# Kernel optimization log

Measured on AMD Instinct MI355X. Metric: run time of the kernel, lower is better.

## Reference

```python
import jax, jax.numpy as jnp
import numpy as np

N = 50000      # nodes
E = 600000     # directed edges (before self-loops)
IN, HID, OUT = 512, 128, 40
EPS_BN = 1e-5
DROP_P = 0.5   # hardcoded in forward via BernoulliDropout(0.5)

# BinActive: sign() forward, straight-through estimator backward (|x|<=1 gate)
@jax.custom_vjp
def binactive(x):
    return jnp.sign(x)

def _ba_fwd(x):
    return jnp.sign(x), x

def _ba_bwd(x, g):
    return (g * (jnp.abs(x) <= 1.0).astype(g.dtype),)

binactive.defvjp(_ba_fwd, _ba_bwd)


def setup_inputs() -> dict:
    key = jax.random.key(0)
    ks = jax.random.split(key, 8)
    x = jax.random.normal(ks[0], (N, IN), dtype=jnp.float32)
    edge_index = jax.random.randint(ks[1], (2, E), 0, N, dtype=jnp.int64)
    w0 = jax.random.normal(ks[2], (IN, HID), dtype=jnp.float32) * 0.05
    b0 = jnp.zeros((HID,), jnp.float32)
    w1 = jax.random.normal(ks[3], (HID, HID), dtype=jnp.float32) * 0.05
    b1 = jnp.zeros((HID,), jnp.float32)
    w2 = jax.random.normal(ks[4], (HID, OUT), dtype=jnp.float32) * 0.05
    b2 = jnp.zeros((OUT,), jnp.float32)
    return {"x": x, "edge_index": edge_index,
            "w0": w0, "b0": b0, "w1": w1, "b1": b1, "w2": w2, "b2": b2}


def _gcn_norm(edge_index):
    # add self-loops, compute symmetric normalization deg^-1/2 A deg^-1/2
    loops = jnp.arange(N, dtype=edge_index.dtype)
    row = jnp.concatenate([edge_index[0], loops])  # destinations
    col = jnp.concatenate([edge_index[1], loops])  # sources
    deg = jax.ops.segment_sum(jnp.ones_like(row, dtype=jnp.float32), row, num_segments=N)
    dinv = jnp.where(deg > 0, deg ** -0.5, 0.0)
    norm = dinv[row] * dinv[col]                   # [E+N]
    return row, col, norm


def _gcn_conv(x, w, b, row, col, norm):
    # binarized weight: sign(w) scaled by mean(|w|) (XNOR-style)
    wb = binactive(w) * jnp.mean(jnp.abs(w))
    h = x @ wb                                     # [N, out]
    msg = h[col] * norm[:, None]                   # gather + scale
    agg = jax.ops.segment_sum(msg, row, num_segments=N)
    return agg + b


def reference(x, edge_index, w0, b0, w1, b1, w2, b2):
    # BatchNorm1d(affine=False), training-mode batch stats over nodes
    mean = jnp.mean(x, axis=0)
    var = jnp.var(x, axis=0)
    h = (x - mean) / jnp.sqrt(var + EPS_BN)

    row, col, norm = _gcn_norm(edge_index)
    dkey = jax.random.key(42)
    weights = [(w0, b0), (w1, b1), (w2, b2)]
    n_layers = len(weights)
    for i, (w, b) in enumerate(weights):
        h = binactive(h)
        h = _gcn_conv(h, w, b, row, col, norm)
        if i != n_layers - 1:  # BernoulliDropout(0.5)
            mask = jax.random.bernoulli(jax.random.fold_in(dkey, i), 1.0 - DROP_P, h.shape)
            h = h * mask.astype(h.dtype) * (1.0 / (1.0 - DROP_P))
    return jax.nn.log_softmax(h, axis=1)
```

## Files before the change

### kernel.cpp

```cpp
#include <hip/hip_runtime.h>
#include <stdint.h>
#include <stddef.h>

#define NN 50000
#define NE 600000
#define DI 512
#define DH 128
#define DO 40
#define MTOT (NN * DH)
#define NBLK ((NN + 255) / 256)
#define CSB 400
#define GEMMB ((NN / 16 + 3) / 4)
#define DEG4B ((NE / 4 + 255) / 256)

using int4v = __attribute__((ext_vector_type(4))) int;

__host__ __device__ inline uint32_t rotl32(uint32_t v, int d) {
  return (v << d) | (v >> (32 - d));
}

__host__ __device__ inline void threefry2x32(uint32_t k0, uint32_t k1,
                                             uint32_t c0, uint32_t c1,
                                             uint32_t* o0, uint32_t* o1) {
  uint32_t ks0 = k0, ks1 = k1, ks2 = k0 ^ k1 ^ 0x1BD11BDAu;
  uint32_t x0 = c0 + ks0, x1 = c1 + ks1;
  const int R0[4] = {13, 15, 26, 6};
  const int R1[4] = {17, 29, 16, 24};
#define TF_R4(R) { x0 += x1; x1 = rotl32(x1, R[0]); x1 ^= x0; \
                   x0 += x1; x1 = rotl32(x1, R[1]); x1 ^= x0; \
                   x0 += x1; x1 = rotl32(x1, R[2]); x1 ^= x0; \
                   x0 += x1; x1 = rotl32(x1, R[3]); x1 ^= x0; }
  TF_R4(R0); x0 += ks1; x1 += ks2 + 1u;
  TF_R4(R1); x0 += ks2; x1 += ks0 + 2u;
  TF_R4(R0); x0 += ks0; x1 += ks1 + 3u;
  TF_R4(R1); x0 += ks1; x1 += ks2 + 4u;
  TF_R4(R0); x0 += ks2; x1 += ks0 + 5u;
#undef TF_R4
  *o0 = x0; *o1 = x1;
}

__device__ inline void colsum_body(const float* __restrict__ x,
                                   double* __restrict__ colsum, int blk) {
  const int t = threadIdx.x;
  const int grp = blk >> 1;
  const int col = ((blk & 1) << 8) + t;
  const float* xp = x + (size_t)grp * 250 * DI + col;
  double s = 0.0;
  for (int i = 0; i < 10; ++i) {
    float f0  = xp[0 * DI],  f1  = xp[1 * DI],  f2  = xp[2 * DI];
    float f3  = xp[3 * DI],  f4  = xp[4 * DI],  f5  = xp[5 * DI];
    float f6  = xp[6 * DI],  f7  = xp[7 * DI],  f8  = xp[8 * DI];
    float f9  = xp[9 * DI],  f10 = xp[10 * DI], f11 = xp[11 * DI];
    float f12 = xp[12 * DI], f13 = xp[13 * DI], f14 = xp[14 * DI];
    float f15 = xp[15 * DI], f16 = xp[16 * DI], f17 = xp[17 * DI];
    float f18 = xp[18 * DI], f19 = xp[19 * DI], f20 = xp[20 * DI];
    float f21 = xp[21 * DI], f22 = xp[22 * DI], f23 = xp[23 * DI];
    float f24 = xp[24 * DI];
    asm volatile("" :: "v"(f0), "v"(f1), "v"(f2), "v"(f3), "v"(f4),
                       "v"(f5), "v"(f6), "v"(f7), "v"(f8), "v"(f9),
                       "v"(f10), "v"(f11), "v"(f12), "v"(f13), "v"(f14),
                       "v"(f15), "v"(f16), "v"(f17), "v"(f18), "v"(f19),
                       "v"(f20), "v"(f21), "v"(f22), "v"(f23), "v"(f24));
    s += (double)f0;  s += (double)f1;  s += (double)f2;  s += (double)f3;
    s += (double)f4;  s += (double)f5;  s += (double)f6;  s += (double)f7;
    s += (double)f8;  s += (double)f9;  s += (double)f10; s += (double)f11;
    s += (double)f12; s += (double)f13; s += (double)f14; s += (double)f15;
    s += (double)f16; s += (double)f17; s += (double)f18; s += (double)f19;
    s += (double)f20; s += (double)f21; s += (double)f22; s += (double)f23;
    s += (double)f24;
    xp += 25 * DI;
  }
  unsafeAtomicAdd(&colsum[col], s);
}

__device__ inline void wfuse_body(const float* __restrict__ w,
                                  uint32_t* __restrict__ frag,
                                  double* __restrict__ slot,
                                  int K, int C, int NT, int blk,
                                  double* red) {
  int steps = K >> 6;
  int total = steps * NT * 64 * 4;
  int idx = blk * 256 + threadIdx.x;
  double a = 0.0;
  if (idx < total) {
    int dw = idx & 3;
    int lane = (idx >> 2) & 63;
    int rest = idx >> 8;
    int t = rest % NT;
    int s = rest / NT;
    int n = t * 16 + (lane & 15);
    int kbase = s * 64 + (lane >> 4) * 16 + dw * 4;
    uint32_t v = 0;
    if (n < C) {
#pragma unroll
      for (int j = 0; j < 4; ++j) {
        float wv = w[(size_t)(kbase + j) * C + n];
        uint32_t sg = (uint8_t)(int8_t)((wv > 0.f) ? 1 : ((wv < 0.f) ? -1 : 0));
        v |= sg << (8 * j);
        a += (double)fabsf(wv);
      }
    }
    frag[idx] = v;
  }
  red[threadIdx.x] = a;
  __syncthreads();
  for (int ofs = 128; ofs > 0; ofs >>= 1) {
    if (threadIdx.x < ofs) red[threadIdx.x] += red[threadIdx.x + ofs];
    __syncthreads();
  }
  if (threadIdx.x == 0) unsafeAtomicAdd(slot, red[0]);
}

__global__ void prologue_fused(const float* __restrict__ x,
                               double* __restrict__ colsum,
                               const int* __restrict__ ei,
                               uint32_t* __restrict__ deg,
                               const float* __restrict__ w0,
                               const float* __restrict__ w1,
                               const float* __restrict__ w2,
                               uint32_t* __restrict__ f0,
                               uint32_t* __restrict__ f1,
                               uint32_t* __restrict__ f2,
                               double* __restrict__ slots) {
  __shared__ double red[256];
  int b = blockIdx.x;
  if (b < CSB) {
    colsum_body(x, colsum, b);
  } else if (b < CSB + DEG4B) {
    int idx = (b - CSB) * 256 + threadIdx.x;
    if (idx < NE / 4) {
      int4 d4 = *(const int4*)(ei + 4 * idx);
      atomicAdd(&deg[d4.x], 1u);
      atomicAdd(&deg[d4.y], 1u);
      atomicAdd(&deg[d4.z], 1u);
      atomicAdd(&deg[d4.w], 1u);
    }
  } else {
    int wb = b - (CSB + DEG4B);
    if (wb < 64)       wfuse_body(w0, f0, slots + 0, DI, DH, 8, wb,      red);
    else if (wb < 80)  wfuse_body(w1, f1, slots + 1, DH, DH, 8, wb - 64, red);
    else               wfuse_body(w2, f2, slots + 2, DH, DO, 3, wb - 80, red);
  }
}

__global__ void scan_mean(const uint32_t* __restrict__ deg,
                          uint32_t* __restrict__ rowptr,
                          uint32_t* __restrict__ bsum,
                          double* __restrict__ dinv,
                          double* __restrict__ colsum) {
  __shared__ uint32_t bs[256];
  int b = blockIdx.x;
  int t = threadIdx.x;
  if (b < NBLK) {
    int i = b * 256 + t;
    uint32_t v = (i < NN) ? deg[i] : 0u;
    if (i < NN) dinv[i] = 1.0 / sqrt((double)(v + 1u));
    bs[t] = v;
    __syncthreads();
    for (int ofs = 1; ofs < 256; ofs <<= 1) {
      uint32_t add = (t >= ofs) ? bs[t - ofs] : 0u;
      __syncthreads();
      bs[t] += add;
      __syncthreads();
    }
    if (i < NN) rowptr[i] = bs[t] - v;
    if (t == 255) bsum[b] = bs[255];
  } else {
    int c = (b - NBLK) * 256 + t;
    if (c < DI) colsum[c] = colsum[c] / (double)NN;
  }
}

__global__ void scan_bsum(const uint32_t* __restrict__ bsum,
                          uint32_t* __restrict__ base) {
  __shared__ uint32_t bs[256];
  int t = threadIdx.x;
  uint32_t v = (t < NBLK) ? bsum[t] : 0u;
  bs[t] = v;
  __syncthreads();
  for (int ofs = 1; ofs < 256; ofs <<= 1) {
    uint32_t add = (t >= ofs) ? bs[t - ofs] : 0u;
    __syncthreads();
    bs[t] += add;
    __syncthreads();
  }
  if (t < NBLK) base[t] = bs[t] - v;
}

__global__ void csr_gemm0(const int* __restrict__ ei,
                          const uint32_t* __restrict__ rowptr,
                          const uint32_t* __restrict__ base,
                          uint32_t* __restrict__ cursor,
                          int* __restrict__ csr_src,
                          const float* __restrict__ x,
                          const double* __restrict__ mean,
                          const uint32_t* __restrict__ frag,
                          int8_t* __restrict__ H) {
  if (blockIdx.x < DEG4B) {
    int idx = blockIdx.x * 256 + threadIdx.x;
    if (idx < NE / 4) {
      int4 d4 = *(const int4*)(ei + 4 * idx);
      int4 s4 = *(const int4*)(ei + NE + 4 * idx);
      uint32_t p0 = rowptr[d4.x] + base[d4.x >> 8] + atomicAdd(&cursor[d4.x], 1u);
      uint32_t p1 = rowptr[d4.y] + base[d4.y >> 8] + atomicAdd(&cursor[d4.y], 1u);
      uint32_t p2 = rowptr[d4.z] + base[d4.z >> 8] + atomicAdd(&cursor[d4.z], 1u);
      uint32_t p3 = rowptr[d4.w] + base[d4.w >> 8] + atomicAdd(&cursor[d4.w], 1u);
      csr_src[p0] = s4.x;
      csr_src[p1] = s4.y;
      csr_src[p2] = s4.z;
      csr_src[p3] = s4.w;
    }
    return;
  }
  const int blk = blockIdx.x - DEG4B;
  const uint4* fg = (const uint4*)frag;
  const int lane = threadIdx.x & 63;
  const int wv = threadIdx.x >> 6;
  const int r0 = (blk * 4 + wv) * 16;
  if (r0 >= NN) return;
  const int m = lane & 15, q = lane >> 4;
  const float* xp = x + (size_t)(r0 + m) * DI + q * 16;
  const double* mp0 = mean + q * 16;
  int4v acc[8];
#pragma unroll
  for (int t = 0; t < 8; ++t) acc[t] = (int4v){0, 0, 0, 0};
#pragma unroll
  for (int s = 0; s < 8; ++s) {
    const float* xs = xp + s * 64;
    const double* mp = mp0 + s * 64;
    int4v a;
#pragma unroll
    for (int w4 = 0; w4 < 4; ++w4) {
      float4 f = *(const float4*)(xs + 4 * w4);
      double v0 = (double)f.x - mp[4 * w4 + 0];
      double v1 = (double)f.y - mp[4 * w4 + 1];
      double v2 = (double)f.z - mp[4 * w4 + 2];
      double v3 = (double)f.w - mp[4 * w4 + 3];
      uint32_t o = 0;
      o |= (uint8_t)(int8_t)((v0 > 0.0) ? 1 : ((v0 < 0.0) ? -1 : 0));
      o |= ((uint32_t)(uint8_t)(int8_t)((v1 > 0.0) ? 1 : ((v1 < 0.0) ? -1 : 0))) << 8;
      o |= ((uint32_t)(uint8_t)(int8_t)((v2 > 0.0) ? 1 : ((v2 < 0.0) ? -1 : 0))) << 16;
      o |= ((uint32_t)(uint8_t)(int8_t)((v3 > 0.0) ? 1 : ((v3 < 0.0) ? -1 : 0))) << 24;
      a[w4] = (int)o;
    }
#pragma unroll
    for (int t = 0; t < 8; ++t) {
      int4v b = *(const int4v*)&fg[(s * 8 + t) * 64 + lane];
      acc[t] = __builtin_amdgcn_mfma_i32_16x16x64_i8(a, b, acc[t], 0, 0, 0);
    }
  }
  int8_t* hp = H + (size_t)r0 * DH;
#pragma unroll
  for (int t = 0; t < 8; ++t) {
    int n = t * 16 + m;
#pragma unroll
    for (int r = 0; r < 4; ++r)
      hp[(size_t)(q * 4 + r) * DH + n] = (int8_t)(acc[t][r] >> 1);
  }
}

template <int STEPS, int NT, int C, int SHIFT>
__global__ void gemm_mfma(const int8_t* __restrict__ S,
                          const uint32_t* __restrict__ frag,
                          int8_t* __restrict__ H) {
  extern __shared__ uint4 lb[];
  const int tot = STEPS * NT * 64;
  const uint4* fg = (const uint4*)frag;
  for (int i = threadIdx.x; i < tot; i += 256) lb[i] = fg[i];
  __syncthreads();
  const int lane = threadIdx.x & 63;
  const int wv = threadIdx.x >> 6;
  const int r0 = (blockIdx.x * 4 + wv) * 16;
  if (r0 >= NN) return;
  const int m = lane & 15, q = lane >> 4;
  const int K = STEPS * 64;
  const int8_t* sp = S + (size_t)(r0 + m) * K + q * 16;
  int4v acc[NT];
#pragma unroll
  for (int t = 0; t < NT; ++t) acc[t] = (int4v){0, 0, 0, 0};
#pragma unroll
  for (int s = 0; s < STEPS; ++s) {
    int4v a = *(const int4v*)(sp + (size_t)s * 64);
#pragma unroll
    for (int t = 0; t < NT; ++t) {
      int4v b = *(const int4v*)&lb[(s * NT + t) * 64 + lane];
      acc[t] = __builtin_amdgcn_mfma_i32_16x16x64_i8(a, b, acc[t], 0, 0, 0);
    }
  }
  int8_t* hp = H + (size_t)r0 * C;
#pragma unroll
  for (int t = 0; t < NT; ++t) {
    int n = t * 16 + m;
    if (n < C) {
#pragma unroll
      for (int r = 0; r < 4; ++r)
        hp[(size_t)(q * 4 + r) * C + n] = (int8_t)(acc[t][r] >> SHIFT);
    }
  }
}

__global__ void gather128(const uint32_t* __restrict__ rowptr,
                          const uint32_t* __restrict__ base,
                          const int* __restrict__ csr_src,
                          const double* __restrict__ dinv,
                          const int8_t* __restrict__ H,
                          const float* __restrict__ b,
                          int8_t* __restrict__ Sout,
                          const double* __restrict__ wsum, double cnt,
                          uint32_t fk0, uint32_t fk1) {
  int d = (int)(((size_t)blockIdx.x * blockDim.x + threadIdx.x) >> 6);
  int lane = threadIdx.x & 63;
  if (d >= NN) return;
  const int g = lane >> 5, p = lane & 31;
  double a0 = 0.0, a1 = 0.0, a2 = 0.0, a3 = 0.0;
  const uint32_t e0 = rowptr[d] + base[d >> 8];
  const uint32_t e1 = (d + 1 < NN) ? (rowptr[d + 1] + base[(d + 1) >> 8]) : NE;
  const int L = (int)(e1 - e0) + 1;
  for (int c0 = 0; c0 < L; c0 += 64) {
    const int n = min(64, L - c0);
    const int my = c0 + lane;
    int sidx = d;
    if (my > 0 && my < L) sidx = csr_src[e0 + my - 1];
    double wv = dinv[sidx];
    int t = 0;
    {
      int sA = 0, sB = 0; double wA = 0.0, wB = 0.0;
      uint32_t hA = 0, hB = 0;
      if (4 <= n) {
        sA = __shfl(sidx, g);      wA = __shfl(wv, g);
        sB = __shfl(sidx, 2 + g);  wB = __shfl(wv, 2 + g);
        hA = *(const uint32_t*)(H + (size_t)sA * DH + 4 * p);
        hB = *(const uint32_t*)(H + (size_t)sB * DH + 4 * p);
      }
      for (; t + 4 <= n; t += 4) {
        const uint32_t cA = hA, cB = hB;
        const double vA = wA, vB = wB;
        if (t + 8 <= n) {
          sA = __shfl(sidx, t + 4 + g);  wA = __shfl(wv, t + 4 + g);
          sB = __shfl(sidx, t + 6 + g);  wB = __shfl(wv, t + 6 + g);
          hA = *(const uint32_t*)(H + (size_t)sA * DH + 4 * p);
          hB = *(const uint32_t*)(H + (size_t)sB * DH + 4 * p);
        }
        a0 += vA * (double)(int8_t)(cA);
        a1 += vA * (double)(int8_t)(cA >> 8);
        a2 += vA * (double)(int8_t)(cA >> 16);
        a3 += vA * (double)(int8_t)(cA >> 24);
        a0 += vB * (double)(int8_t)(cB);
        a1 += vB * (double)(int8_t)(cB >> 8);
        a2 += vB * (double)(int8_t)(cB >> 16);
        a3 += vB * (double)(int8_t)(cB >> 24);
      }
    }
    for (; t < n; t += 2) {
      const int j = t + g;
      const bool on = (j < n);
      const int jc = on ? j : 0;
      int s = __shfl(sidx, jc);
      double w = __shfl(wv, jc);
      w = on ? w : 0.0;
      uint32_t hv = *(const uint32_t*)(H + (size_t)s * DH + 4 * p);
      a0 += w * (double)(int8_t)(hv);
      a1 += w * (double)(int8_t)(hv >> 8);
      a2 += w * (double)(int8_t)(hv >> 16);
      a3 += w * (double)(int8_t)(hv >> 24);
    }
  }
  a0 += __shfl_xor(a0, 32);
  a1 += __shfl_xor(a1, 32);
  a2 += __shfl_xor(a2, 32);
  a3 += __shfl_xor(a3, 32);
  double sc = (wsum[0] / cnt) * dinv[d];
  int ch = 4 * p + 2 * g;
  int j0 = d * DH + ch;
  double va = sc * ((g == 0) ? a0 : a2) + (double)b[ch];
  double vb = sc * ((g == 0) ? a1 : a3) + (double)b[ch + 1];
  int s0 = (va > 0.0) ? 1 : ((va < 0.0) ? -1 : 0);
  int s1 = (vb > 0.0) ? 1 : ((vb < 0.0) ? -1 : 0);
  uint32_t r0, r1, bits0, bits1;
  threefry2x32(fk0, fk1, 0u, (uint32_t)j0, &r0, &r1);
  bits0 = r0 ^ r1;
  threefry2x32(fk0, fk1, 0u, (uint32_t)(j0 + 1), &r0, &r1);
  bits1 = r0 ^ r1;
  float u0 = __uint_as_float((bits0 >> 9) | 0x3f800000u) - 1.0f;
  float u1 = __uint_as_float((bits1 >> 9) | 0x3f800000u) - 1.0f;
  uint8_t o0 = (u0 < 0.5f) ? (uint8_t)(int8_t)s0 : (uint8_t)0;
  uint8_t o1 = (u1 < 0.5f) ? (uint8_t)(int8_t)s1 : (uint8_t)0;
  *(uint16_t*)(Sout + j0) = (uint16_t)(o0 | ((uint16_t)o1 << 8));
}

__global__ void gather40_lsm(const uint32_t* __restrict__ rowptr,
                             const uint32_t* __restrict__ base,
                             const int* __restrict__ csr_src,
                             const double* __restrict__ dinv,
                             const int8_t* __restrict__ H,
                             const float* __restrict__ b2,
                             const double* __restrict__ wsum,
                             float* __restrict__ out) {
  int d = (int)(((size_t)blockIdx.x * blockDim.x + threadIdx.x) >> 6);
  int lane = threadIdx.x & 63;
  if (d >= NN) return;
  const int g = lane >> 5, p = lane & 31;
  const bool act = (p < 20);
  double a0 = 0.0, a1 = 0.0;
  const uint32_t e0 = rowptr[d] + base[d >> 8];
  const uint32_t e1 = (d + 1 < NN) ? (rowptr[d + 1] + base[(d + 1) >> 8]) : NE;
  const int L = (int)(e1 - e0) + 1;
  for (int c0 = 0; c0 < L; c0 += 64) {
    const int n = min(64, L - c0);
    const int my = c0 + lane;
    int sidx = d;
    if (my > 0 && my < L) sidx = csr_src[e0 + my - 1];
    double wv = dinv[sidx];
    int t = 0;
    {
      int sA = 0, sB = 0; double wA = 0.0, wB = 0.0;
      uint16_t hA = 0, hB = 0;
      if (4 <= n) {
        sA = __shfl(sidx, g);      wA = __shfl(wv, g);
        sB = __shfl(sidx, 2 + g);  wB = __shfl(wv, 2 + g);
        if (act) {
          hA = *(const uint16_t*)(H + (size_t)sA * DO + 2 * p);
          hB = *(const uint16_t*)(H + (size_t)sB * DO + 2 * p);
        }
      }
      for (; t + 4 <= n; t += 4) {
        const uint16_t cA = hA, cB = hB;
        const double vA = wA, vB = wB;
        if (t + 8 <= n) {
          sA = __shfl(sidx, t + 4 + g);  wA = __shfl(wv, t + 4 + g);
          sB = __shfl(sidx, t + 6 + g);  wB = __shfl(wv, t + 6 + g);
          if (act) {
            hA = *(const uint16_t*)(H + (size_t)sA * DO + 2 * p);
            hB = *(const uint16_t*)(H + (size_t)sB * DO + 2 * p);
          }
        }
        if (act) {
          a0 += vA * (double)(int8_t)(cA);
          a1 += vA * (double)(int8_t)(cA >> 8);
          a0 += vB * (double)(int8_t)(cB);
          a1 += vB * (double)(int8_t)(cB >> 8);
        }
      }
    }
    for (; t < n; t += 2) {
      const int j = t + g;
      const bool on = (j < n);
      const int jc = on ? j : 0;
      int s = __shfl(sidx, jc);
      double w = __shfl(wv, jc);
      w = on ? w : 0.0;
      if (act) {
        uint16_t hv = *(const uint16_t*)(H + (size_t)s * DO + 2 * p);
        a0 += w * (double)(int8_t)(hv);
        a1 += w * (double)(int8_t)(hv >> 8);
      }
    }
  }
  a0 += __shfl_xor(a0, 32);
  a1 += __shfl_xor(a1, 32);
  double sc = (wsum[0] / (double)(DH * DO)) * dinv[d];
  const bool lead = (g == 0) && act;
  double v0 = 0.0, v1 = 0.0;
  if (act) {
    v0 = sc * a0 + (double)b2[2 * p];
    v1 = sc * a1 + (double)b2[2 * p + 1];
  }
  double mx = lead ? fmax(v0, v1) : -1.0e300;
  for (int ofs = 32; ofs > 0; ofs >>= 1) mx = fmax(mx, __shfl_xor(mx, ofs));
  float ex = lead ? (expf((float)(v0 - mx)) + expf((float)(v1 - mx))) : 0.f;
  for (int ofs = 32; ofs > 0; ofs >>= 1) ex += __shfl_xor(ex, ofs);
  float l = logf(ex);
  if (lead) {
    float2 o = make_float2((float)(v0 - mx) - l, (float)(v1 - mx) - l);
    *(float2*)(out + (size_t)d * DO + 2 * p) = o;
  }
}

extern "C" void kernel_launch(void* const* d_in, const int* in_sizes, int n_in,
                              void* d_out, int out_size, void* d_ws, size_t ws_size,
                              hipStream_t stream) {
  (void)in_sizes; (void)n_in; (void)out_size; (void)ws_size;
  const float* x  = (const float*)d_in[0];
  const int*   ei = (const int*)d_in[1];
  const float* w0 = (const float*)d_in[2];
  const float* b0 = (const float*)d_in[3];
  const float* w1 = (const float*)d_in[4];
  const float* b1 = (const float*)d_in[5];
  const float* w2 = (const float*)d_in[6];
  const float* b2 = (const float*)d_in[7];
  float* out = (float*)d_out;

  char* wsb = (char*)d_ws;
  double*   mean_d = (double*)wsb;
  double*   wsum_d = (double*)(wsb + 4096);
  uint32_t* deg_e  = (uint32_t*)(wsb + 4224);
  uint32_t* cursor = (uint32_t*)(wsb + 204224);
  size_t cur = 404480;
  uint32_t* rowptr = (uint32_t*)(wsb + cur); cur += 200064;
  double*   dinv_d = (double*)(wsb + cur);  cur += 400000;
  cur = (cur + 255) & ~255ull;
  uint32_t* bsum = (uint32_t*)(wsb + cur); cur += 1024;
  uint32_t* base = (uint32_t*)(wsb + cur); cur += 1024;
  int*    csr_src = (int*)(wsb + cur);    cur += (size_t)NE * 4;
  cur = (cur + 255) & ~255ull;
  uint32_t* FR0 = (uint32_t*)(wsb + cur); cur += 8 * 8 * 64 * 16;
  uint32_t* FR1 = (uint32_t*)(wsb + cur); cur += 2 * 8 * 64 * 16;
  uint32_t* FR2 = (uint32_t*)(wsb + cur); cur += 2 * 3 * 64 * 16;
  int8_t* S1  = (int8_t*)(wsb + cur); cur += (size_t)MTOT;
  cur = (cur + 255) & ~255ull;
  int8_t* H8 = (int8_t*)(wsb + cur); cur += (size_t)MTOT;

  uint32_t fkA0, fkA1, fkB0, fkB1;
  threefry2x32(0u, 42u, 0u, 0u, &fkA0, &fkA1);
  threefry2x32(0u, 42u, 0u, 1u, &fkB0, &fkB1);

  hipMemsetAsync(wsb, 0, 404224, stream);

  prologue_fused<<<CSB + DEG4B + 86, 256, 0, stream>>>(
      x, mean_d, ei, deg_e, w0, w1, w2, FR0, FR1, FR2, wsum_d);
  scan_mean<<<NBLK + 2, 256, 0, stream>>>(deg_e, rowptr, bsum, dinv_d, mean_d);
  scan_bsum<<<1, 256, 0, stream>>>(bsum, base);

  const int node_blocks = (NN * 64) / 256 + 1;
  const size_t sh1 = 2 * 8 * 64 * 16;
  const size_t sh2 = 2 * 3 * 64 * 16;

  csr_gemm0<<<DEG4B + GEMMB, 256, 0, stream>>>(ei, rowptr, base, cursor,
                                               csr_src, x, mean_d, FR0, H8);
  gather128<<<node_blocks, 256, 0, stream>>>(rowptr, base, csr_src, dinv_d, H8,
                                             b0, S1, wsum_d + 0,
                                             (double)(DI * DH / 2), fkA0, fkA1);

  gemm_mfma<2, 8, DH, 0><<<GEMMB, 256, sh1, stream>>>(S1, FR1, H8);
  gather128<<<node_blocks, 256, 0, stream>>>(rowptr, base, csr_src, dinv_d, H8,
                                             b1, S1, wsum_d + 1,
                                             (double)(DH * DH), fkB0, fkB1);

  gemm_mfma<2, 3, DO, 0><<<GEMMB, 256, sh2, stream>>>(S1, FR2, H8);
  gather40_lsm<<<node_blocks, 256, 0, stream>>>(rowptr, base, csr_src, dinv_d,
                                                H8, b2, wsum_d + 2, out);
}
```

Baseline: 369.4 us.

## Prefetch x rows in GEMM, hoist dropout RNG, load dinv per edge directly

In the int8 MFMA GEMM fused with BN-sign, x rows are loaded into a four-stage register buffer ahead of use, so global loads overlap the sign/pack and MFMA work. In gather128, the threefry dropout bits are computed before the edge loop so that ALU work can overlap the first memory latencies. In both gather kernels, the per-edge dinv weight is now read from memory (a uniform address per half-wave) instead of being broadcast with a double-precision shuffle, which removes shuffle instructions but adds dependent loads. Register pressure rises from the prefetch buffer and the hoisted RNG values.

```diff
diff --git a/kernel.cpp b/kernel.cpp
--- a/kernel.cpp
+++ b/kernel.cpp
@@ -221,21 +221,34 @@
   const int m = lane & 15, q = lane >> 4;
   const float* xp = x + (size_t)(r0 + m) * DI + q * 16;
   const double* mp0 = mean + q * 16;
+  float4 buf[4][4];
+#pragma unroll
+  for (int s = 0; s < 4; ++s)
+#pragma unroll
+    for (int w = 0; w < 4; ++w)
+      buf[s][w] = *(const float4*)(xp + s * 64 + 4 * w);
   int4v acc[8];
 #pragma unroll
   for (int t = 0; t < 8; ++t) acc[t] = (int4v){0, 0, 0, 0};
 #pragma unroll
   for (int s = 0; s < 8; ++s) {
-    const float* xs = xp + s * 64;
+    float4 f[4];
+#pragma unroll
+    for (int w = 0; w < 4; ++w) f[w] = buf[s & 3][w];
+    if (s + 4 < 8) {
+#pragma unroll
+      for (int w = 0; w < 4; ++w)
+        buf[s & 3][w] = *(const float4*)(xp + (s + 4) * 64 + 4 * w);
+    }
     const double* mp = mp0 + s * 64;
     int4v a;
 #pragma unroll
     for (int w4 = 0; w4 < 4; ++w4) {
-      float4 f = *(const float4*)(xs + 4 * w4);
-      double v0 = (double)f.x - mp[4 * w4 + 0];
-      double v1 = (double)f.y - mp[4 * w4 + 1];
-      double v2 = (double)f.z - mp[4 * w4 + 2];
-      double v3 = (double)f.w - mp[4 * w4 + 3];
+      float4 fv = f[w4];
+      double v0 = (double)fv.x - mp[4 * w4 + 0];
+      double v1 = (double)fv.y - mp[4 * w4 + 1];
+      double v2 = (double)fv.z - mp[4 * w4 + 2];
+      double v3 = (double)fv.w - mp[4 * w4 + 3];
       uint32_t o = 0;
       o |= (uint8_t)(int8_t)((v0 > 0.0) ? 1 : ((v0 < 0.0) ? -1 : 0));
       o |= ((uint32_t)(uint8_t)(int8_t)((v1 > 0.0) ? 1 : ((v1 < 0.0) ? -1 : 0))) << 8;
@@ -312,6 +325,15 @@
   int lane = threadIdx.x & 63;
   if (d >= NN) return;
   const int g = lane >> 5, p = lane & 31;
+  const int ch = 4 * p + 2 * g;
+  const int j0 = d * DH + ch;
+  uint32_t r0_, r1_, bits0, bits1;
+  threefry2x32(fk0, fk1, 0u, (uint32_t)j0, &r0_, &r1_);
+  bits0 = r0_ ^ r1_;
+  threefry2x32(fk0, fk1, 0u, (uint32_t)(j0 + 1), &r0_, &r1_);
+  bits1 = r0_ ^ r1_;
+  float u0 = __uint_as_float((bits0 >> 9) | 0x3f800000u) - 1.0f;
+  float u1 = __uint_as_float((bits1 >> 9) | 0x3f800000u) - 1.0f;
   double a0 = 0.0, a1 = 0.0, a2 = 0.0, a3 = 0.0;
   const uint32_t e0 = rowptr[d] + base[d >> 8];
   const uint32_t e1 = (d + 1 < NN) ? (rowptr[d + 1] + base[(d + 1) >> 8]) : NE;
@@ -321,14 +343,13 @@
     const int my = c0 + lane;
     int sidx = d;
     if (my > 0 && my < L) sidx = csr_src[e0 + my - 1];
-    double wv = dinv[sidx];
     int t = 0;
     {
       int sA = 0, sB = 0; double wA = 0.0, wB = 0.0;
       uint32_t hA = 0, hB = 0;
       if (4 <= n) {
-        sA = __shfl(sidx, g);      wA = __shfl(wv, g);
-        sB = __shfl(sidx, 2 + g);  wB = __shfl(wv, 2 + g);
+        sA = __shfl(sidx, g);      sB = __shfl(sidx, 2 + g);
+        wA = dinv[sA];             wB = dinv[sB];
         hA = *(const uint32_t*)(H + (size_t)sA * DH + 4 * p);
         hB = *(const uint32_t*)(H + (size_t)sB * DH + 4 * p);
       }
@@ -336,8 +357,8 @@
         const uint32_t cA = hA, cB = hB;
         const double vA = wA, vB = wB;
         if (t + 8 <= n) {
-          sA = __shfl(sidx, t + 4 + g);  wA = __shfl(wv, t + 4 + g);
-          sB = __shfl(sidx, t + 6 + g);  wB = __shfl(wv, t + 6 + g);
+          sA = __shfl(sidx, t + 4 + g);  sB = __shfl(sidx, t + 6 + g);
+          wA = dinv[sA];                 wB = dinv[sB];
           hA = *(const uint32_t*)(H + (size_t)sA * DH + 4 * p);
           hB = *(const uint32_t*)(H + (size_t)sB * DH + 4 * p);
         }
@@ -356,8 +377,7 @@
       const bool on = (j < n);
       const int jc = on ? j : 0;
       int s = __shfl(sidx, jc);
-      double w = __shfl(wv, jc);
-      w = on ? w : 0.0;
+      double w = on ? dinv[s] : 0.0;
       uint32_t hv = *(const uint32_t*)(H + (size_t)s * DH + 4 * p);
       a0 += w * (double)(int8_t)(hv);
       a1 += w * (double)(int8_t)(hv >> 8);
@@ -370,19 +390,10 @@
   a2 += __shfl_xor(a2, 32);
   a3 += __shfl_xor(a3, 32);
   double sc = (wsum[0] / cnt) * dinv[d];
-  int ch = 4 * p + 2 * g;
-  int j0 = d * DH + ch;
   double va = sc * ((g == 0) ? a0 : a2) + (double)b[ch];
   double vb = sc * ((g == 0) ? a1 : a3) + (double)b[ch + 1];
   int s0 = (va > 0.0) ? 1 : ((va < 0.0) ? -1 : 0);
   int s1 = (vb > 0.0) ? 1 : ((vb < 0.0) ? -1 : 0);
-  uint32_t r0, r1, bits0, bits1;
-  threefry2x32(fk0, fk1, 0u, (uint32_t)j0, &r0, &r1);
-  bits0 = r0 ^ r1;
-  threefry2x32(fk0, fk1, 0u, (uint32_t)(j0 + 1), &r0, &r1);
-  bits1 = r0 ^ r1;
-  float u0 = __uint_as_float((bits0 >> 9) | 0x3f800000u) - 1.0f;
-  float u1 = __uint_as_float((bits1 >> 9) | 0x3f800000u) - 1.0f;
   uint8_t o0 = (u0 < 0.5f) ? (uint8_t)(int8_t)s0 : (uint8_t)0;
   uint8_t o1 = (u1 < 0.5f) ? (uint8_t)(int8_t)s1 : (uint8_t)0;
   *(uint16_t*)(Sout + j0) = (uint16_t)(o0 | ((uint16_t)o1 << 8));
@@ -410,14 +421,13 @@
     const int my = c0 + lane;
     int sidx = d;
     if (my > 0 && my < L) sidx = csr_src[e0 + my - 1];
-    double wv = dinv[sidx];
     int t = 0;
     {
       int sA = 0, sB = 0; double wA = 0.0, wB = 0.0;
       uint16_t hA = 0, hB = 0;
       if (4 <= n) {
-        sA = __shfl(sidx, g);      wA = __shfl(wv, g);
-        sB = __shfl(sidx, 2 + g);  wB = __shfl(wv, 2 + g);
+        sA = __shfl(sidx, g);      sB = __shfl(sidx, 2 + g);
+        wA = dinv[sA];             wB = dinv[sB];
         if (act) {
           hA = *(const uint16_t*)(H + (size_t)sA * DO + 2 * p);
           hB = *(const uint16_t*)(H + (size_t)sB * DO + 2 * p);
@@ -427,8 +437,8 @@
         const uint16_t cA = hA, cB = hB;
         const double vA = wA, vB = wB;
         if (t + 8 <= n) {
-          sA = __shfl(sidx, t + 4 + g);  wA = __shfl(wv, t + 4 + g);
-          sB = __shfl(sidx, t + 6 + g);  wB = __shfl(wv, t + 6 + g);
+          sA = __shfl(sidx, t + 4 + g);  sB = __shfl(sidx, t + 6 + g);
+          wA = dinv[sA];                 wB = dinv[sB];
           if (act) {
             hA = *(const uint16_t*)(H + (size_t)sA * DO + 2 * p);
             hB = *(const uint16_t*)(H + (size_t)sB * DO + 2 * p);
@@ -447,8 +457,7 @@
       const bool on = (j < n);
       const int jc = on ? j : 0;
       int s = __shfl(sidx, jc);
-      double w = __shfl(wv, jc);
-      w = on ? w : 0.0;
+      double w = on ? dinv[s] : 0.0;
       if (act) {
         uint16_t hv = *(const uint16_t*)(H + (size_t)s * DO + 2 * p);
         a0 += w * (double)(int8_t)(hv);
```

New measurement: 371.1 us. Within noise of the previous version (+0.5%).
